# Performance work log

Hardware: AMD Instinct MI355X
Metric: run time of the kernel (lower is better)

The kernel has to match this reference:

```python
import jax, jax.numpy as jnp
import numpy as np

SIGMA_NEU = 0.05
SIGMA_SYN = 0.002
NOISE_START = 16  # torch: noise added when t > 15
ALPHA_TS = 0.25
BETA_TS = 0.1


def setup_inputs() -> dict:
    key = jax.random.key(0)
    ks = jax.random.split(key, 6)
    B, T, n_in, n_hid, n_out = 32, 64, 64, 512, 16
    inp = {}
    inp["input_signal"] = jax.random.normal(ks[0], (B, T, n_in), jnp.float32)
    inp["hidden"] = jax.random.normal(ks[1], (B, n_hid), jnp.float32) * 0.1
    inp["w_in"] = jax.random.normal(ks[2], (n_hid, n_in), jnp.float32) / np.sqrt(n_in)
    inp["w_hh"] = jax.random.normal(ks[3], (n_hid, n_hid), jnp.float32) / np.sqrt(n_hid)
    inp["b_hh"] = jax.random.normal(ks[4], (n_hid,), jnp.float32) * 0.01
    inp["w_out"] = jax.random.normal(ks[5], (n_out, n_hid), jnp.float32) / np.sqrt(n_hid)
    inp["alpha"] = jnp.full((n_hid,), ALPHA_TS, jnp.float32)
    inp["beta"] = jnp.full((n_hid,), BETA_TS, jnp.float32)
    return inp


def reference(input_signal, hidden, w_in, w_hh, b_hh, w_out, alpha, beta):
    B, T, _ = input_signal.shape
    n_hid = hidden.shape[1]
    x = jnp.transpose(input_signal, (1, 0, 2))  # [T, B, n_in]
    base = jax.random.key(1234)
    sqrt_a = jnp.sqrt(alpha)
    sqrt_b = jnp.sqrt(beta)
    new_j0 = jnp.broadcast_to(w_hh, (B, n_hid, n_hid))  # new_j starts at w_hh

    def step(carry, xs):
        h, new_j = carry
        t, x_t = xs
        k1, k2 = jax.random.split(jax.random.fold_in(base, t))
        a = jnp.tanh(h)
        diff_j = new_j - w_hh  # [B, n_hid, n_hid] plastic deviation
        dj_act = jnp.einsum('bi,bij->bj', a, diff_j)
        tmp = x_t @ w_in.T + a @ w_hh.T + b_hh + dj_act
        neu = jax.random.normal(k1, h.shape, h.dtype) * SIGMA_NEU * sqrt_a
        gate = jnp.where(t >= NOISE_START, jnp.float32(1.0), jnp.float32(0.0))
        h = (1.0 - alpha) * h + alpha * tmp + gate * neu
        # anti-Hebbian rank-1 update + synaptic noise (beta broadcasts over last dim)
        syn = jax.random.normal(k2, new_j.shape, new_j.dtype) * SIGMA_SYN * sqrt_b
        add_w = -jnp.einsum('bi,bj->bij', a, a) + syn
        new_j = new_j + beta * add_w
        out = h @ w_out.T
        return (h, new_j), (h, out)

    (hidden, new_j), (hl, ol) = jax.lax.scan(step, (hidden, new_j0), (jnp.arange(T), x))
    hidden_list = jnp.transpose(hl, (1, 0, 2))  # [B, T, n_hid]
    output_list = jnp.transpose(ol, (1, 0, 2))  # [B, T, n_out]
    return hidden_list, output_list, hidden, new_j
```

## Files before the change

### kernel.cpp

```cpp
#include <hip/hip_runtime.h>

#define B_SZ 32
#define T_STEPS 64
#define N_IN 64
#define N_HID 512
#define N_OUT 16
#define NOISE_START_T 16

#define WGS 256
#define WPB 32
#define JPW 16
#define NWG (B_SZ * WPB)

#define HL_OFF  0
#define OL_OFF  (B_SZ * T_STEPS * N_HID)
#define HID_OFF (OL_OFF + B_SZ * T_STEPS * N_OUT)
#define NJ_OFF  (HID_OFF + B_SZ * N_HID)

#define CNT_BYTES 4096

typedef float v2f __attribute__((ext_vector_type(2)));

__device__ __forceinline__ void tf2x32(unsigned k0, unsigned k1, unsigned x0, unsigned x1,
                                       unsigned& o0, unsigned& o1) {
  unsigned ks2 = k0 ^ k1 ^ 0x1BD11BDAu;
#define TFR(r) { x0 += x1; x1 = (x1 << (r)) | (x1 >> (32 - (r))); x1 ^= x0; }
  x0 += k0; x1 += k1;
  TFR(13) TFR(15) TFR(26) TFR(6)
  x0 += k1; x1 += ks2 + 1u;
  TFR(17) TFR(29) TFR(16) TFR(24)
  x0 += ks2; x1 += k0 + 2u;
  TFR(13) TFR(15) TFR(26) TFR(6)
  x0 += k0; x1 += k1 + 3u;
  TFR(17) TFR(29) TFR(16) TFR(24)
  x0 += k1; x1 += ks2 + 4u;
  TFR(13) TFR(15) TFR(26) TFR(6)
  x0 += ks2; x1 += k0 + 5u;
#undef TFR
  o0 = x0; o1 = x1;
}

__device__ __forceinline__ unsigned rbits(unsigned kx, unsigned ky, unsigned n) {
  unsigned a, b; tf2x32(kx, ky, 0u, n, a, b); return a ^ b;
}

__device__ __forceinline__ float nrm_from_bits(unsigned bits) {
  const float lo = -0.99999994039535522461f;
  float f = __uint_as_float((bits >> 9) | 0x3F800000u) - 1.0f;
  float u = fmaxf(lo, f * 2.0f + lo);
  float w = -__logf((1.0f - u) * (1.0f + u));
  float p;
  if (w < 5.0f) {
    w -= 2.5f;
    p =            2.81022636e-08f;
    p = fmaf(p, w, 3.43273939e-07f);
    p = fmaf(p, w, -3.5233877e-06f);
    p = fmaf(p, w, -4.39150654e-06f);
    p = fmaf(p, w, 0.00021858087f);
    p = fmaf(p, w, -0.00125372503f);
    p = fmaf(p, w, -0.00417768164f);
    p = fmaf(p, w, 0.246640727f);
    p = fmaf(p, w, 1.50140941f);
  } else {
    w = sqrtf(w) - 3.0f;
    p =            -0.000200214257f;
    p = fmaf(p, w, 0.000100950558f);
    p = fmaf(p, w, 0.00134934322f);
    p = fmaf(p, w, -0.00367342844f);
    p = fmaf(p, w, 0.00573950773f);
    p = fmaf(p, w, -0.0076224613f);
    p = fmaf(p, w, 0.00943887047f);
    p = fmaf(p, w, 1.00167406f);
    p = fmaf(p, w, 2.83297682f);
  }
  return 1.41421356f * (p * u);
}

__device__ __forceinline__ void pubf(float* p, float v) {
  __hip_atomic_store(p, v, __ATOMIC_RELAXED, __HIP_MEMORY_SCOPE_AGENT);
}
__device__ __forceinline__ v2f rd2(const float* p) {
  unsigned long long raw = __hip_atomic_load((const unsigned long long*)p,
                                             __ATOMIC_RELAXED, __HIP_MEMORY_SCOPE_AGENT);
  v2f r; __builtin_memcpy(&r, &raw, 8); return r;
}

__global__ __launch_bounds__(WGS) __attribute__((amdgpu_waves_per_eu(4, 4)))
void rnn_fused(
    const float* __restrict__ x, const float* __restrict__ h0_in,
    const float* __restrict__ w_in, const float* __restrict__ w_hh,
    const float* __restrict__ b_hh, const float* __restrict__ w_out,
    const float* __restrict__ alpha, const float* __restrict__ beta,
    float* __restrict__ out, float* __restrict__ wsf, unsigned* __restrict__ cnts) {
  __shared__ __align__(16) unsigned char smem[40960];
  float* d_lds   = (float*)smem;
  float* a_lds   = (float*)(smem + 32768);
  float* xw_lds  = (float*)(smem + 34816);
  unsigned* keyl = (unsigned*)(smem + 38912);
  float* olred   = (float*)(smem + 39936);

  const int tid = threadIdx.x;
  const int b   = blockIdx.x >> 5;
  const int blk = blockIdx.x & 31;
  const int jl  = tid >> 4;
  const int ib  = tid & 15;
  const int jg  = blk * JPW + jl;
  const bool leader = (ib == 0);

  float* hl  = out + HL_OFF;
  float* ol  = out + OL_OFF;
  float* hid = out + HID_OFF;
  float* nj  = out + NJ_OFF + (size_t)b * (N_HID * N_HID);
  unsigned* cnt = cnts + (size_t)b * 32;
  float* hex  = wsf;
  float* aexb = wsf + 2 * B_SZ * N_HID;

  if (tid < T_STEPS) {
    unsigned f0, f1, a0, a1, b0, b1;
    tf2x32(0u, 1234u, 0u, (unsigned)tid, f0, f1);
    tf2x32(f0, f1, 0u, 0u, a0, a1);
    tf2x32(f0, f1, 0u, 1u, b0, b1);
    keyl[tid * 4 + 0] = a0; keyl[tid * 4 + 1] = a1;
    keyl[tid * 4 + 2] = b0; keyl[tid * 4 + 3] = b1;
  }
#pragma unroll
  for (int k = 0; k < 32; ++k) d_lds[k * 256 + tid] = 0.f;
#pragma unroll
  for (int r = 0; r < 4; ++r) {
    int m = r * 256 + tid;
    int tt = m >> 4, jj = m & 15;
    const float* xr = x + ((size_t)b * T_STEPS + tt) * N_IN;
    const float* wr = w_in + (size_t)(blk * JPW + jj) * N_IN;
    float s = 0.f;
#pragma unroll
    for (int k = 0; k < N_IN; ++k) s = fmaf(xr[k], wr[k], s);
    xw_lds[tt * JPW + jj] = s;
  }
  a_lds[tid]       = tanhf(h0_in[b * N_HID + tid]);
  a_lds[tid + 256] = tanhf(h0_in[b * N_HID + tid + 256]);

  const float* whrow = w_hh + (size_t)jg * N_HID;
  const float bet = beta[jg];
  const float sb  = sqrtf(bet);
  const float al  = alpha[jg];
  const float sqa = sqrtf(al);
  const float bh  = b_hh[jg];
  float h_reg = h0_in[b * N_HID + jg];

  __syncthreads();

  unsigned target = 0;
  const unsigned nb = (unsigned)(b * N_HID * N_HID) + (unsigned)jg;

  for (int t = 0; t < T_STEPS; ++t) {
    const int q = (t + 1) & 1;
    const unsigned k1x = __builtin_amdgcn_readfirstlane(keyl[t * 4 + 0]);
    const unsigned k1y = __builtin_amdgcn_readfirstlane(keyl[t * 4 + 1]);
    const unsigned k2x = __builtin_amdgcn_readfirstlane(keyl[t * 4 + 2]);
    const unsigned k2y = __builtin_amdgcn_readfirstlane(keyl[t * 4 + 3]);
    const float ajg = a_lds[jg];

    float accd = 0.f, accw = 0.f;
#pragma unroll
    for (int k = 0; k < 8; ++k) {
      const int i = k * 64 + ib * 4;
      float4 av = *(const float4*)&a_lds[i];
      float4 wv = *(const float4*)&whrow[i];
      float d0 = d_lds[(k * 4 + 0) * 256 + tid];
      float d1 = d_lds[(k * 4 + 1) * 256 + tid];
      float d2 = d_lds[(k * 4 + 2) * 256 + tid];
      float d3 = d_lds[(k * 4 + 3) * 256 + tid];
      accw = fmaf(av.x, wv.x, accw); accw = fmaf(av.y, wv.y, accw);
      accw = fmaf(av.z, wv.z, accw); accw = fmaf(av.w, wv.w, accw);
      accd = fmaf(av.x, d0, accd); accd = fmaf(av.y, d1, accd);
      accd = fmaf(av.z, d2, accd); accd = fmaf(av.w, d3, accd);
      const unsigned n = nb + (unsigned)i * 512u;
      float z0 = nrm_from_bits(rbits(k2x, k2y, n));
      float z1 = nrm_from_bits(rbits(k2x, k2y, n + 512u));
      float z2 = nrm_from_bits(rbits(k2x, k2y, n + 1024u));
      float z3 = nrm_from_bits(rbits(k2x, k2y, n + 1536u));
      d_lds[(k * 4 + 0) * 256 + tid] = d0 + bet * ((z0 * 0.002f) * sb - av.x * ajg);
      d_lds[(k * 4 + 1) * 256 + tid] = d1 + bet * ((z1 * 0.002f) * sb - av.y * ajg);
      d_lds[(k * 4 + 2) * 256 + tid] = d2 + bet * ((z2 * 0.002f) * sb - av.z * ajg);
      d_lds[(k * 4 + 3) * 256 + tid] = d3 + bet * ((z3 * 0.002f) * sb - av.w * ajg);
    }
#pragma unroll
    for (int m = 1; m < 16; m <<= 1) {
      accd += __shfl_xor(accd, m);
      accw += __shfl_xor(accw, m);
    }

    if (leader) {
      const float xw = xw_lds[t * JPW + jl];
      float tmp = ((xw + accw) + bh) + accd;
      float hn = (1.f - al) * h_reg + al * tmp;
      if (t >= NOISE_START_T) {
        unsigned m0 = (unsigned)(b * N_HID + jg);
        hn += (nrm_from_bits(rbits(k1x, k1y, m0)) * 0.05f) * sqa;
      }
      h_reg = hn;
      float an = tanhf(hn);
      pubf(hex  + (size_t)(q * B_SZ + b) * N_HID + jg, hn);
      pubf(aexb + (size_t)(q * B_SZ + b) * N_HID + jg, an);
      hl[((size_t)b * T_STEPS + t) * N_HID + jg] = hn;
      if (t == T_STEPS - 1) hid[b * N_HID + jg] = hn;
    }

    __syncthreads();
    target += WPB;
    if (tid == 0) {
      __hip_atomic_fetch_add(cnt, 1u, __ATOMIC_RELAXED, __HIP_MEMORY_SCOPE_AGENT);
      while (__hip_atomic_load(cnt, __ATOMIC_RELAXED, __HIP_MEMORY_SCOPE_AGENT) < target)
        __builtin_amdgcn_s_sleep(1);
    }
    __builtin_amdgcn_sched_barrier(0);
    __syncthreads();

    {
      const float* aq = aexb + (size_t)(q * B_SZ + b) * N_HID;
      v2f av = rd2(aq + 2 * tid);
      a_lds[2 * tid] = av.x; a_lds[2 * tid + 1] = av.y;
    }
    __syncthreads();

    if (blk == 0) {
      const float* hq = hex + (size_t)(q * B_SZ + b) * N_HID;
      const int o = tid & 15, qq = tid >> 4;
      const float* wo = w_out + o * N_HID;
      float p = 0.f;
#pragma unroll
      for (int m2 = 0; m2 < 16; ++m2) {
        v2f hv = rd2(hq + qq * 32 + 2 * m2);
        p = fmaf(hv.x, wo[qq * 32 + 2 * m2], p);
        p = fmaf(hv.y, wo[qq * 32 + 2 * m2 + 1], p);
      }
      olred[tid] = p;
      __syncthreads();
      if (tid < N_OUT) {
        float s = 0.f;
#pragma unroll
        for (int m = 0; m < 16; ++m) s += olred[m * 16 + tid];
        ol[((size_t)b * T_STEPS + t) * N_OUT + tid] = s;
      }
    }
  }

  __syncthreads();
  {
    const int jj = tid & 15;
#pragma unroll
    for (int g = 0; g < 32; ++g) {
      const int i = g * 16 + (tid >> 4);
      const int k = i >> 6, e = i & 3, ibb = (i >> 2) & 15;
      const float dv = d_lds[(k * 4 + e) * 256 + jj * 16 + ibb];
      const size_t o = (size_t)i * N_HID + blk * JPW + jj;
      nj[o] = dv + w_hh[o];
    }
  }
}

extern "C" void kernel_launch(void* const* d_in, const int* in_sizes, int n_in,
                              void* d_out, int out_size, void* d_ws, size_t ws_size,
                              hipStream_t stream) {
  const float* x     = (const float*)d_in[0];
  const float* h0    = (const float*)d_in[1];
  const float* win   = (const float*)d_in[2];
  const float* whh   = (const float*)d_in[3];
  const float* bhh   = (const float*)d_in[4];
  const float* wout  = (const float*)d_in[5];
  const float* alpha = (const float*)d_in[6];
  const float* beta  = (const float*)d_in[7];
  (void)in_sizes; (void)n_in; (void)out_size; (void)ws_size;

  hipMemsetAsync(d_ws, 0, CNT_BYTES, stream);
  unsigned* cnts = (unsigned*)d_ws;
  float* wsf = (float*)((char*)d_ws + CNT_BYTES);
  rnn_fused<<<NWG, WGS, 0, stream>>>(x, h0, win, whh, bhh, wout, alpha, beta,
                                     (float*)d_out, wsf, cnts);
}
```

Measured before the change: 1.760 ms.

## Double workgroup size to 512 threads, halving per-thread plastic-weight elements

Raises threads per workgroup from 256 to 512 so each thread handles 16 elements of the plastic deviation matrix instead of 32, with a 32-lane reduction per output neuron. This spreads the per-step RNG and FMA work across more waves to shorten each recurrent step's critical path. The precomputed input projection moves from LDS to a global workspace buffer, and the a-vector load and output reduction are reshaped to match. Costs include a longer shuffle reduction, more waves contending at the per-step barriers, and scalar rather than float4 loads.

```diff
diff --git a/kernel.cpp b/kernel.cpp
--- a/kernel.cpp
+++ b/kernel.cpp
@@ -7,9 +7,10 @@
 #define N_OUT 16
 #define NOISE_START_T 16
 
-#define WGS 256
+#define WGS 512
 #define WPB 32
 #define JPW 16
+#define EPT 16
 #define NWG (B_SZ * WPB)
 
 #define HL_OFF  0
@@ -18,6 +19,9 @@
 #define NJ_OFF  (HID_OFF + B_SZ * N_HID)
 
 #define CNT_BYTES 4096
+#define HEX_OFF 0
+#define AEX_OFF (2 * B_SZ * N_HID)
+#define XWG_OFF (4 * B_SZ * N_HID)
 
 typedef float v2f __attribute__((ext_vector_type(2)));
 
@@ -79,31 +83,33 @@
 __device__ __forceinline__ void pubf(float* p, float v) {
   __hip_atomic_store(p, v, __ATOMIC_RELAXED, __HIP_MEMORY_SCOPE_AGENT);
 }
+__device__ __forceinline__ float rdf(const float* p) {
+  return __hip_atomic_load(p, __ATOMIC_RELAXED, __HIP_MEMORY_SCOPE_AGENT);
+}
 __device__ __forceinline__ v2f rd2(const float* p) {
   unsigned long long raw = __hip_atomic_load((const unsigned long long*)p,
                                              __ATOMIC_RELAXED, __HIP_MEMORY_SCOPE_AGENT);
   v2f r; __builtin_memcpy(&r, &raw, 8); return r;
 }
 
-__global__ __launch_bounds__(WGS) __attribute__((amdgpu_waves_per_eu(4, 4)))
+__global__ __launch_bounds__(WGS) __attribute__((amdgpu_waves_per_eu(8, 8)))
 void rnn_fused(
     const float* __restrict__ x, const float* __restrict__ h0_in,
     const float* __restrict__ w_in, const float* __restrict__ w_hh,
     const float* __restrict__ b_hh, const float* __restrict__ w_out,
     const float* __restrict__ alpha, const float* __restrict__ beta,
     float* __restrict__ out, float* __restrict__ wsf, unsigned* __restrict__ cnts) {
-  __shared__ __align__(16) unsigned char smem[40960];
+  __shared__ __align__(16) unsigned char smem[37888];
   float* d_lds   = (float*)smem;
   float* a_lds   = (float*)(smem + 32768);
-  float* xw_lds  = (float*)(smem + 34816);
-  unsigned* keyl = (unsigned*)(smem + 38912);
-  float* olred   = (float*)(smem + 39936);
+  unsigned* keyl = (unsigned*)(smem + 34816);
+  float* olred   = (float*)(smem + 35840);
 
   const int tid = threadIdx.x;
   const int b   = blockIdx.x >> 5;
   const int blk = blockIdx.x & 31;
-  const int jl  = tid >> 4;
-  const int ib  = tid & 15;
+  const int jl  = tid >> 5;
+  const int ib  = tid & 31;
   const int jg  = blk * JPW + jl;
   const bool leader = (ib == 0);
 
@@ -112,8 +118,9 @@
   float* hid = out + HID_OFF;
   float* nj  = out + NJ_OFF + (size_t)b * (N_HID * N_HID);
   unsigned* cnt = cnts + (size_t)b * 32;
-  float* hex  = wsf;
-  float* aexb = wsf + 2 * B_SZ * N_HID;
+  float* hex  = wsf + HEX_OFF;
+  float* aexb = wsf + AEX_OFF;
+  float* xwg  = wsf + XWG_OFF + (size_t)blockIdx.x * (T_STEPS * JPW);
 
   if (tid < T_STEPS) {
     unsigned f0, f1, a0, a1, b0, b1;
@@ -124,22 +131,21 @@
     keyl[tid * 4 + 2] = b0; keyl[tid * 4 + 3] = b1;
   }
 #pragma unroll
-  for (int k = 0; k < 32; ++k) d_lds[k * 256 + tid] = 0.f;
-#pragma unroll
-  for (int r = 0; r < 4; ++r) {
-    int m = r * 256 + tid;
+  for (int e = 0; e < EPT; ++e) d_lds[e * 512 + tid] = 0.f;
+#pragma unroll
+  for (int r = 0; r < 2; ++r) {
+    int m = r * 512 + tid;
     int tt = m >> 4, jj = m & 15;
     const float* xr = x + ((size_t)b * T_STEPS + tt) * N_IN;
     const float* wr = w_in + (size_t)(blk * JPW + jj) * N_IN;
     float s = 0.f;
 #pragma unroll
     for (int k = 0; k < N_IN; ++k) s = fmaf(xr[k], wr[k], s);
-    xw_lds[tt * JPW + jj] = s;
-  }
-  a_lds[tid]       = tanhf(h0_in[b * N_HID + tid]);
-  a_lds[tid + 256] = tanhf(h0_in[b * N_HID + tid + 256]);
-
-  const float* whrow = w_hh + (size_t)jg * N_HID;
+    xwg[m] = s;
+  }
+  a_lds[tid] = tanhf(h0_in[b * N_HID + tid]);
+
+  const float* wcol = w_hh + (size_t)jg * N_HID;
   const float bet = beta[jg];
   const float sb  = sqrtf(bet);
   const float al  = alpha[jg];
@@ -162,36 +168,24 @@
 
     float accd = 0.f, accw = 0.f;
 #pragma unroll
-    for (int k = 0; k < 8; ++k) {
-      const int i = k * 64 + ib * 4;
-      float4 av = *(const float4*)&a_lds[i];
-      float4 wv = *(const float4*)&whrow[i];
-      float d0 = d_lds[(k * 4 + 0) * 256 + tid];
-      float d1 = d_lds[(k * 4 + 1) * 256 + tid];
-      float d2 = d_lds[(k * 4 + 2) * 256 + tid];
-      float d3 = d_lds[(k * 4 + 3) * 256 + tid];
-      accw = fmaf(av.x, wv.x, accw); accw = fmaf(av.y, wv.y, accw);
-      accw = fmaf(av.z, wv.z, accw); accw = fmaf(av.w, wv.w, accw);
-      accd = fmaf(av.x, d0, accd); accd = fmaf(av.y, d1, accd);
-      accd = fmaf(av.z, d2, accd); accd = fmaf(av.w, d3, accd);
-      const unsigned n = nb + (unsigned)i * 512u;
-      float z0 = nrm_from_bits(rbits(k2x, k2y, n));
-      float z1 = nrm_from_bits(rbits(k2x, k2y, n + 512u));
-      float z2 = nrm_from_bits(rbits(k2x, k2y, n + 1024u));
-      float z3 = nrm_from_bits(rbits(k2x, k2y, n + 1536u));
-      d_lds[(k * 4 + 0) * 256 + tid] = d0 + bet * ((z0 * 0.002f) * sb - av.x * ajg);
-      d_lds[(k * 4 + 1) * 256 + tid] = d1 + bet * ((z1 * 0.002f) * sb - av.y * ajg);
-      d_lds[(k * 4 + 2) * 256 + tid] = d2 + bet * ((z2 * 0.002f) * sb - av.z * ajg);
-      d_lds[(k * 4 + 3) * 256 + tid] = d3 + bet * ((z3 * 0.002f) * sb - av.w * ajg);
-    }
-#pragma unroll
-    for (int m = 1; m < 16; m <<= 1) {
+    for (int e = 0; e < EPT; ++e) {
+      const int i = e * 32 + ib;
+      const float av = a_lds[i];
+      const float wv = wcol[i];
+      const float dv = d_lds[e * 512 + tid];
+      accw = fmaf(av, wv, accw);
+      accd = fmaf(av, dv, accd);
+      const float z = nrm_from_bits(rbits(k2x, k2y, nb + (unsigned)i * 512u));
+      d_lds[e * 512 + tid] = dv + bet * ((z * 0.002f) * sb - av * ajg);
+    }
+#pragma unroll
+    for (int m = 1; m < 32; m <<= 1) {
       accd += __shfl_xor(accd, m);
       accw += __shfl_xor(accw, m);
     }
 
     if (leader) {
-      const float xw = xw_lds[t * JPW + jl];
+      const float xw = xwg[t * JPW + jl];
       float tmp = ((xw + accw) + bh) + accd;
       float hn = (1.f - al) * h_reg + al * tmp;
       if (t >= NOISE_START_T) {
@@ -216,11 +210,7 @@
     __builtin_amdgcn_sched_barrier(0);
     __syncthreads();
 
-    {
-      const float* aq = aexb + (size_t)(q * B_SZ + b) * N_HID;
-      v2f av = rd2(aq + 2 * tid);
-      a_lds[2 * tid] = av.x; a_lds[2 * tid + 1] = av.y;
-    }
+    a_lds[tid] = rdf(aexb + (size_t)(q * B_SZ + b) * N_HID + tid);
     __syncthreads();
 
     if (blk == 0) {
@@ -229,17 +219,17 @@
       const float* wo = w_out + o * N_HID;
       float p = 0.f;
 #pragma unroll
-      for (int m2 = 0; m2 < 16; ++m2) {
-        v2f hv = rd2(hq + qq * 32 + 2 * m2);
-        p = fmaf(hv.x, wo[qq * 32 + 2 * m2], p);
-        p = fmaf(hv.y, wo[qq * 32 + 2 * m2 + 1], p);
+      for (int m2 = 0; m2 < 8; ++m2) {
+        v2f hv = rd2(hq + qq * 16 + 2 * m2);
+        p = fmaf(hv.x, wo[qq * 16 + 2 * m2], p);
+        p = fmaf(hv.y, wo[qq * 16 + 2 * m2 + 1], p);
       }
       olred[tid] = p;
       __syncthreads();
       if (tid < N_OUT) {
         float s = 0.f;
 #pragma unroll
-        for (int m = 0; m < 16; ++m) s += olred[m * 16 + tid];
+        for (int m = 0; m < 32; ++m) s += olred[m * 16 + tid];
         ol[((size_t)b * T_STEPS + t) * N_OUT + tid] = s;
       }
     }
@@ -248,11 +238,11 @@
   __syncthreads();
   {
     const int jj = tid & 15;
-#pragma unroll
-    for (int g = 0; g < 32; ++g) {
-      const int i = g * 16 + (tid >> 4);
-      const int k = i >> 6, e = i & 3, ibb = (i >> 2) & 15;
-      const float dv = d_lds[(k * 4 + e) * 256 + jj * 16 + ibb];
+    const int rr = tid >> 4;
+#pragma unroll
+    for (int g = 0; g < 16; ++g) {
+      const int i = g * 32 + rr;
+      const float dv = d_lds[g * 512 + jj * 32 + rr];
       const size_t o = (size_t)i * N_HID + blk * JPW + jj;
       nj[o] = dv + w_hh[o];
     }
```

Measured after the change: 1.924 ms. +9.3%, slower.

## Overlap plastic-weight update and output projection with cross-workgroup barrier wait

Applied to the files above, without the earlier changes.

Moves the anti-Hebbian plus synaptic-noise update of the plastic deviation out of the matvec loop. It now runs after the arrival increment and before the spin-wait on the per-batch counter, so the RNG and LDS update work hides barrier latency. The output projection is delayed by one step and reads from a triple-buffered h exchange, so it also runs inside the wait window. A tail block computes the last step's output. The cost is a second pass over LDS and the a vector, plus more workspace for the three h buffers.

```diff
diff --git a/kernel.cpp b/kernel.cpp
--- a/kernel.cpp
+++ b/kernel.cpp
@@ -18,6 +18,8 @@
 #define NJ_OFF  (HID_OFF + B_SZ * N_HID)
 
 #define CNT_BYTES 4096
+#define HEX_OFF 0
+#define AEX_OFF (3 * B_SZ * N_HID)
 
 typedef float v2f __attribute__((ext_vector_type(2)));
 
@@ -112,8 +114,8 @@
   float* hid = out + HID_OFF;
   float* nj  = out + NJ_OFF + (size_t)b * (N_HID * N_HID);
   unsigned* cnt = cnts + (size_t)b * 32;
-  float* hex  = wsf;
-  float* aexb = wsf + 2 * B_SZ * N_HID;
+  float* hex  = wsf + HEX_OFF;
+  float* aexb = wsf + AEX_OFF;
 
   if (tid < T_STEPS) {
     unsigned f0, f1, a0, a1, b0, b1;
@@ -151,6 +153,7 @@
 
   unsigned target = 0;
   const unsigned nb = (unsigned)(b * N_HID * N_HID) + (unsigned)jg;
+  int hs = 0;
 
   for (int t = 0; t < T_STEPS; ++t) {
     const int q = (t + 1) & 1;
@@ -174,15 +177,6 @@
       accw = fmaf(av.z, wv.z, accw); accw = fmaf(av.w, wv.w, accw);
       accd = fmaf(av.x, d0, accd); accd = fmaf(av.y, d1, accd);
       accd = fmaf(av.z, d2, accd); accd = fmaf(av.w, d3, accd);
-      const unsigned n = nb + (unsigned)i * 512u;
-      float z0 = nrm_from_bits(rbits(k2x, k2y, n));
-      float z1 = nrm_from_bits(rbits(k2x, k2y, n + 512u));
-      float z2 = nrm_from_bits(rbits(k2x, k2y, n + 1024u));
-      float z3 = nrm_from_bits(rbits(k2x, k2y, n + 1536u));
-      d_lds[(k * 4 + 0) * 256 + tid] = d0 + bet * ((z0 * 0.002f) * sb - av.x * ajg);
-      d_lds[(k * 4 + 1) * 256 + tid] = d1 + bet * ((z1 * 0.002f) * sb - av.y * ajg);
-      d_lds[(k * 4 + 2) * 256 + tid] = d2 + bet * ((z2 * 0.002f) * sb - av.z * ajg);
-      d_lds[(k * 4 + 3) * 256 + tid] = d3 + bet * ((z3 * 0.002f) * sb - av.w * ajg);
     }
 #pragma unroll
     for (int m = 1; m < 16; m <<= 1) {
@@ -200,31 +194,35 @@
       }
       h_reg = hn;
       float an = tanhf(hn);
-      pubf(hex  + (size_t)(q * B_SZ + b) * N_HID + jg, hn);
-      pubf(aexb + (size_t)(q * B_SZ + b) * N_HID + jg, an);
+      pubf(hex  + (size_t)(hs * B_SZ + b) * N_HID + jg, hn);
+      pubf(aexb + (size_t)(q  * B_SZ + b) * N_HID + jg, an);
       hl[((size_t)b * T_STEPS + t) * N_HID + jg] = hn;
       if (t == T_STEPS - 1) hid[b * N_HID + jg] = hn;
     }
 
     __syncthreads();
     target += WPB;
-    if (tid == 0) {
+    if (tid == 0)
       __hip_atomic_fetch_add(cnt, 1u, __ATOMIC_RELAXED, __HIP_MEMORY_SCOPE_AGENT);
-      while (__hip_atomic_load(cnt, __ATOMIC_RELAXED, __HIP_MEMORY_SCOPE_AGENT) < target)
-        __builtin_amdgcn_s_sleep(1);
-    }
-    __builtin_amdgcn_sched_barrier(0);
-    __syncthreads();
-
-    {
-      const float* aq = aexb + (size_t)(q * B_SZ + b) * N_HID;
-      v2f av = rd2(aq + 2 * tid);
-      a_lds[2 * tid] = av.x; a_lds[2 * tid + 1] = av.y;
-    }
-    __syncthreads();
-
-    if (blk == 0) {
-      const float* hq = hex + (size_t)(q * B_SZ + b) * N_HID;
+
+#pragma unroll
+    for (int k = 0; k < 8; ++k) {
+      const int i = k * 64 + ib * 4;
+      float4 av = *(const float4*)&a_lds[i];
+      const unsigned n = nb + (unsigned)i * 512u;
+      float z0 = nrm_from_bits(rbits(k2x, k2y, n));
+      float z1 = nrm_from_bits(rbits(k2x, k2y, n + 512u));
+      float z2 = nrm_from_bits(rbits(k2x, k2y, n + 1024u));
+      float z3 = nrm_from_bits(rbits(k2x, k2y, n + 1536u));
+      d_lds[(k * 4 + 0) * 256 + tid] += bet * ((z0 * 0.002f) * sb - av.x * ajg);
+      d_lds[(k * 4 + 1) * 256 + tid] += bet * ((z1 * 0.002f) * sb - av.y * ajg);
+      d_lds[(k * 4 + 2) * 256 + tid] += bet * ((z2 * 0.002f) * sb - av.z * ajg);
+      d_lds[(k * 4 + 3) * 256 + tid] += bet * ((z3 * 0.002f) * sb - av.w * ajg);
+    }
+
+    if (blk == 0 && t > 0) {
+      const int ps = (hs == 0) ? 2 : hs - 1;
+      const float* hq = hex + (size_t)(ps * B_SZ + b) * N_HID;
       const int o = tid & 15, qq = tid >> 4;
       const float* wo = w_out + o * N_HID;
       float p = 0.f;
@@ -240,8 +238,44 @@
         float s = 0.f;
 #pragma unroll
         for (int m = 0; m < 16; ++m) s += olred[m * 16 + tid];
-        ol[((size_t)b * T_STEPS + t) * N_OUT + tid] = s;
+        ol[((size_t)b * T_STEPS + (t - 1)) * N_OUT + tid] = s;
       }
+    }
+
+    if (tid == 0) {
+      while (__hip_atomic_load(cnt, __ATOMIC_RELAXED, __HIP_MEMORY_SCOPE_AGENT) < target)
+        __builtin_amdgcn_s_sleep(1);
+    }
+    __builtin_amdgcn_sched_barrier(0);
+    __syncthreads();
+    {
+      const float* aq = aexb + (size_t)(q * B_SZ + b) * N_HID;
+      v2f av = rd2(aq + 2 * tid);
+      a_lds[2 * tid] = av.x; a_lds[2 * tid + 1] = av.y;
+    }
+    __syncthreads();
+
+    hs = (hs == 2) ? 0 : hs + 1;
+  }
+
+  if (blk == 0) {
+    const float* hq = hex + (size_t)(((T_STEPS - 1) % 3) * B_SZ + b) * N_HID;
+    const int o = tid & 15, qq = tid >> 4;
+    const float* wo = w_out + o * N_HID;
+    float p = 0.f;
+#pragma unroll
+    for (int m2 = 0; m2 < 16; ++m2) {
+      v2f hv = rd2(hq + qq * 32 + 2 * m2);
+      p = fmaf(hv.x, wo[qq * 32 + 2 * m2], p);
+      p = fmaf(hv.y, wo[qq * 32 + 2 * m2 + 1], p);
+    }
+    olred[tid] = p;
+    __syncthreads();
+    if (tid < N_OUT) {
+      float s = 0.f;
+#pragma unroll
+      for (int m = 0; m < 16; ++m) s += olred[m * 16 + tid];
+      ol[((size_t)b * T_STEPS + (T_STEPS - 1)) * N_OUT + tid] = s;
     }
   }
 
```

New measurement: 1.594 ms. -9.4%, faster.
